# Optimization experiments

Hardware: AMD Instinct MI355X
Metric: run time of the kernel (lower is better)

## Reference

```python
import jax, jax.numpy as jnp
import numpy as np
import math

D_MODEL = 256
NUM_HEADS = 8
K_NEIGHBORS = 16


def sine_pos_embedding(pos_xy, d_model):
    # Faithful to PositionalEncoding: pos_xy [B, N, 2] -> [B, N, d_model]
    half = d_model // 2
    dim_t = jnp.arange(half, dtype=jnp.float32)
    dim_t = 10000.0 ** (2.0 * jnp.floor(dim_t / 2.0) / half)
    recip = (2.0 * math.pi) / dim_t  # [half]
    px = pos_xy[:, :, 0, None] * recip  # [B, N, half]
    py = pos_xy[:, :, 1, None] * recip
    def interleave(p):
        s = jnp.sin(p[:, :, 0::2])
        c = jnp.cos(p[:, :, 1::2])
        return jnp.stack((s, c), axis=3).reshape(p.shape[0], p.shape[1], -1)
    return jnp.concatenate((interleave(py), interleave(px)), axis=2)


def knn_indices(pos, K, valid_mask):
    # Faithful to find_k_nearest_neighbors: cdist, mask invalid ROWS with +inf, topk smallest.
    # pos: [B, N, 3], valid_mask: [B, N] -> indices [B, N, K]
    sq = jnp.sum(pos * pos, axis=-1)  # [B, N]
    d2 = sq[:, :, None] + sq[:, None, :] - 2.0 * jnp.einsum('bnd,bmd->bnm', pos, pos)
    dist = jnp.sqrt(jnp.maximum(d2, 0.0))  # [B, N, N]
    INF = jnp.float32(np.inf)
    dist = jnp.where(valid_mask[:, :, None], dist, INF)  # torch masks rows via (~mask).unsqueeze(-1)
    _, idx = jax.lax.top_k(-dist, K)  # smallest distances
    return idx  # [B, N, K] int32


def setup_inputs() -> dict:
    key = jax.random.key(0)
    ks = jax.random.split(key, 8)
    B, N, D = 16, 1024, D_MODEL
    x = jax.random.normal(ks[0], (B, N, D), dtype=jnp.float32)
    x_pos = jax.random.normal(ks[1], (B, N, 3), dtype=jnp.float32) * 50.0
    x_mask = jax.random.bernoulli(ks[2], 0.9, (B, N))
    # guarantee at least one valid token per batch row (module asserts sum > 0)
    x_mask = x_mask.at[:, 0].set(True)
    scale = 1.0 / math.sqrt(D)
    Wq = jax.random.normal(ks[3], (D, D), dtype=jnp.float32) * scale
    Wk = jax.random.normal(ks[4], (D, D), dtype=jnp.float32) * scale
    Wv = jax.random.normal(ks[5], (D, D), dtype=jnp.float32) * scale
    Wo = jax.random.normal(ks[6], (D, D), dtype=jnp.float32) * scale
    return {"x": x, "x_pos": x_pos, "x_mask": x_mask,
            "Wq": Wq, "Wk": Wk, "Wv": Wv, "Wo": Wo}


def local_attention(x, pe, valid, idx, Wq, Wk, Wv, Wo):
    B, N, D = x.shape
    H = NUM_HEADS
    dh = D // H
    q = (x + pe) @ Wq  # [B, N, D]
    k = (x + pe) @ Wk
    v = x @ Wv
    # gather K neighbors per query: [B, N, K, D]
    gather = jax.vmap(lambda arr, ii: arr[ii])
    k_n = gather(k, idx)
    v_n = gather(v, idx)
    nbr_valid = gather(valid, idx)  # [B, N, K]
    q = q.reshape(B, N, H, dh)
    k_n = k_n.reshape(B, N, K_NEIGHBORS, H, dh)
    v_n = v_n.reshape(B, N, K_NEIGHBORS, H, dh)
    scores = jnp.einsum('bnhd,bnkhd->bnhk', q, k_n) / math.sqrt(dh)
    scores = jnp.where(nbr_valid[:, :, None, :], scores, jnp.float32(-1e9))
    attn = jax.nn.softmax(scores, axis=-1)
    out = jnp.einsum('bnhk,bnkhd->bnhd', attn, v_n).reshape(B, N, D)
    out = out @ Wo
    out = x + out  # residual
    # zero out invalid tokens, as ret_full_feature is zeros for invalid rows
    return jnp.where(valid[:, :, None], out, 0.0)


def reference(x, x_pos, x_mask, Wq, Wk, Wv, Wo):
    idx = knn_indices(x_pos, K_NEIGHBORS, x_mask)
    pe = sine_pos_embedding(x_pos[:, :, 0:2], D_MODEL)
    pe = jnp.where(x_mask[:, :, None], pe, 0.0)
    return local_attention(x, pe, x_mask, idx, Wq, Wk, Wv, Wo)
```

## Files before the change

### kernel.cpp

```cpp
#include <hip/hip_runtime.h>
#include <math.h>

#define BB 16
#define NN 1024
#define DD 256
#define HH 8
#define DHH 32
#define KNBR 16
#define MM (BB*NN)

typedef __attribute__((ext_vector_type(8))) short  bf16x8;
typedef __attribute__((ext_vector_type(4))) float  f32x4;
typedef __attribute__((ext_vector_type(2))) unsigned short u16x2;
typedef __attribute__((ext_vector_type(4))) unsigned short u16x4;

#define OFF_FLAG 0
#define OFF_XPE  ((size_t)256)
#define OFF_XBF  (OFF_XPE + (size_t)MM*DD*2)
#define OFF_WT   (OFF_XBF + (size_t)MM*DD*2)
#define OFF_Q    (OFF_WT  + (size_t)4*DD*DD*2)
#define OFF_K    (OFF_Q   + (size_t)MM*DD*2)
#define OFF_V    (OFF_K   + (size_t)MM*DD*2)
#define OFF_AO   OFF_XPE
#define OFF_IDX  (OFF_V   + (size_t)MM*DD*2)
#define WS_NEED  (OFF_IDX + (size_t)MM*KNBR*4)

__device__ __forceinline__ float bf2f(unsigned short u) {
    unsigned x = ((unsigned)u) << 16;
    return __builtin_bit_cast(float, x);
}
__device__ __forceinline__ unsigned short f2bf(float f) {
    unsigned x = __builtin_bit_cast(unsigned, f);
    unsigned r = (x + 0x7fffu + ((x >> 16) & 1u)) >> 16;
    return (unsigned short)r;
}
__device__ __forceinline__ int mbcnt64(unsigned long long b) {
    return __builtin_amdgcn_mbcnt_hi((unsigned)(b >> 32),
           __builtin_amdgcn_mbcnt_lo((unsigned)b, 0));
}

__device__ __forceinline__ int get_valid(const void* m, int i, int u8) {
    if (u8) return ((const unsigned char*)m)[i] != 0;
    return ((const unsigned*)m)[i] != 0u;
}

__global__ __launch_bounds__(256, 8) void prep_fused(
    const float* __restrict__ xpos, int* __restrict__ idxout,
    const float* __restrict__ x, const void* __restrict__ mask,
    int* __restrict__ flag,
    const float* __restrict__ Wq, const float* __restrict__ Wk,
    const float* __restrict__ Wv, const float* __restrict__ Wo,
    unsigned short* __restrict__ WT,
    unsigned short* __restrict__ xpebf, unsigned short* __restrict__ xbf) {
    __shared__ float4   sp[NN];
    __shared__ unsigned scand[4][64];
    int bid = blockIdx.x;
    int tid = threadIdx.x;

    if (bid == 0) {
        __shared__ int s_u8, s_f32;
        if (tid == 0) { s_u8 = 0; s_f32 = 0; }
        __syncthreads();
        int u8 = 0, f32 = 0;
        const unsigned* mraw = (const unsigned*)mask;
        for (int i = tid; i < 4096; i += 256) {
            unsigned w = mraw[i];
            if (w == 0x3f800000u) f32 = 1;
            else if (w > 1u) u8 = 1;
        }
        if (u8)  atomicOr(&s_u8, 1);
        if (f32) atomicOr(&s_f32, 1);
        __syncthreads();
        if (tid == 0) *flag = (s_f32 ? 0 : (s_u8 ? 1 : 0));
        return;
    }
    if (bid >= 5121) {
        int pb = bid - 5121;
        int t = pb * 2 + (tid >> 7);
        int p = tid & 127;
        int half = p >> 6;
        int j = p & 63;
        float pos = xpos[(size_t)t*3 + (half ? 0 : 1)];
        float recip = 6.2831853071795864f * exp2f(-(float)j * 0.20762050593045952f);
        float th = pos * recip;
        float s, c;
        __sincosf(th, &s, &c);
        size_t o = (size_t)t*DD + half*128 + 2*j;
        float2 xv = *(const float2*)(x + o);
        u16x2 xb; xb[0] = f2bf(xv.x);     xb[1] = f2bf(xv.y);
        u16x2 xp; xp[0] = f2bf(xv.x + s); xp[1] = f2bf(xv.y + c);
        *(u16x2*)(xbf + o)   = xb;
        *(u16x2*)(xpebf + o) = xp;
        return;
    }
    if (bid >= 4097) {
        int g = bid - 4097;
        int wsel = g >> 8;
        int kk = g & 255;
        const float* W = (wsel == 0) ? Wq : (wsel == 1) ? Wk : (wsel == 2) ? Wv : Wo;
        WT[(size_t)wsel*65536 + (size_t)tid*256 + kk] = f2bf(W[(size_t)kk*256 + tid]);
        return;
    }

    int kb = bid - 1;
    int nblk = kb & 255;
    int b    = kb >> 8;
    for (int i = tid; i < NN; i += 256) {
        const float* p = xpos + ((size_t)b*NN + i)*3;
        float px = p[0], py = p[1], pz = p[2];
        sp[i] = make_float4(px, py, pz, px*px + py*py + pz*pz);
    }
    __syncthreads();
    int wave = tid >> 6, lane = tid & 63;
    int n = nblk * 4 + wave;
    float4 qp = sp[n];
    float d[16];
    #pragma unroll
    for (int t = 0; t < 16; ++t) {
        float4 pm = sp[lane + 64*t];
        float dot = qp.x*pm.x + qp.y*pm.y + qp.z*pm.z;
        float d2 = qp.w + pm.w - 2.f*dot;
        d[t] = fmaxf(d2, 0.f);
    }
    float lmin = d[0];
    #pragma unroll
    for (int t = 1; t < 16; ++t) lmin = fminf(lmin, d[t]);
    float xs = lmin;
    #pragma unroll
    for (int kk = 2; kk <= 64; kk <<= 1) {
        #pragma unroll
        for (int j = kk >> 1; j >= 1; j >>= 1) {
            float vv = __shfl_xor(xs, j);
            bool up = ((lane & kk) == 0);
            bool lower = ((lane & j) == 0);
            xs = (up == lower) ? fminf(xs, vv) : fmaxf(xs, vv);
        }
    }
    float tau = __shfl(xs, 15);
    int T = 0;
    #pragma unroll
    for (int t = 0; t < 16; ++t) T += (d[t] <= tau) ? 1 : 0;
    #pragma unroll
    for (int off = 1; off <= 32; off <<= 1) T += __shfl_xor(T, off);

    bool fast = (T <= 64);
    if (fast) {
        int base = 0;
        #pragma unroll
        for (int t = 0; t < 16; ++t) {
            bool c = (d[t] <= tau);
            unsigned long long bb = __ballot(c);
            if (c) scand[wave][base + mbcnt64(bb)] = __builtin_bit_cast(unsigned, d[t]);
            base += (int)__popcll(bb);
        }
    }
    __syncthreads();

    int out_base = (b*NN + n) * KNBR;
    if (fast) {
        unsigned key = (lane < T) ? scand[wave][lane] : 0xFFFFFFFFu;
        #pragma unroll
        for (int kk = 2; kk <= 64; kk <<= 1) {
            #pragma unroll
            for (int j = kk >> 1; j >= 1; j >>= 1) {
                unsigned vv = (unsigned)__shfl_xor((int)key, j);
                bool up = ((lane & kk) == 0);
                bool lower = ((lane & j) == 0);
                bool takemin = (up == lower);
                key = (takemin == (key < vv)) ? key : vv;
            }
        }
        unsigned tau2 = (unsigned)__shfl((int)key, 15);
        int c1 = (int)__popcll(__ballot(key < tau2));
        int lt_base = 0, eq_seen = 0;
        #pragma unroll
        for (int t = 0; t < 16; ++t) {
            unsigned du = __builtin_bit_cast(unsigned, d[t]);
            bool lt = du < tau2;
            bool eq = du == tau2;
            unsigned long long blt = __ballot(lt);
            unsigned long long beq = __ballot(beq ? eq : eq);
            (void)beq;
            beq = __ballot(eq);
            if (lt) idxout[out_base + lt_base + mbcnt64(blt)] = lane + 64*t;
            int er = eq_seen + mbcnt64(beq);
            if (eq && (c1 + er) < KNBR) idxout[out_base + c1 + er] = lane + 64*t;
            lt_base += (int)__popcll(blt);
            eq_seen += (int)__popcll(beq);
        }
    } else {
        #pragma unroll 1
        for (int it = 0; it < KNBR; ++it) {
            float bd = 3.4e38f; int bm = 1 << 30;
            #pragma unroll
            for (int t = 0; t < 16; ++t)
                if (d[t] < bd) { bd = d[t]; bm = lane + 64*t; }
            #pragma unroll
            for (int off = 32; off >= 1; off >>= 1) {
                float od = __shfl_xor(bd, off);
                int   om = __shfl_xor(bm, off);
                if (od < bd || (od == bd && om < bm)) { bd = od; bm = om; }
            }
            if (lane == 0) idxout[out_base + it] = bm;
            int sel = bm >> 6;
            int mine = ((bm & 63) == lane);
            #pragma unroll
            for (int t = 0; t < 16; ++t)
                if (mine && t == sel) d[t] = 3.4e38f;
        }
    }
}

template<int EPI>
__device__ __forceinline__ void gemm_mfma_core(
    const unsigned short* __restrict__ A, const unsigned short* __restrict__ BT,
    void* __restrict__ C, const float* __restrict__ resid,
    const void* __restrict__ mask, int u8, int bm, int bn, char* smem) {
    unsigned short (*As)[32] = (unsigned short (*)[32])smem;
    unsigned short (*Bs)[32] = (unsigned short (*)[32])(smem + 8192);
    int tid = threadIdx.x;
    int w = tid >> 6, l = tid & 63;
    int wr = w >> 1, wc = w & 1;

    f32x4 acc[4][4] = {};

    for (int kt = 0; kt < 8; ++kt) {
        #pragma unroll
        for (int j = 0; j < 2; ++j) {
            int c  = (w + j*4)*64 + l;
            int row = c >> 2;
            int cb  = (c & 3) * 16;
            const char* ga = (const char*)A + ((size_t)(bm + row)*256 + kt*32)*2 + cb;
            char* la = (char*)As + (size_t)(w + j*4)*1024;
            __builtin_amdgcn_global_load_lds(
                (const __attribute__((address_space(1))) unsigned*)ga,
                (__attribute__((address_space(3))) unsigned*)la, 16, 0, 0);
            const char* gb = (const char*)BT + ((size_t)(bn + row)*256 + kt*32)*2 + cb;
            char* lb = (char*)Bs + (size_t)(w + j*4)*1024;
            __builtin_amdgcn_global_load_lds(
                (const __attribute__((address_space(1))) unsigned*)gb,
                (__attribute__((address_space(3))) unsigned*)lb, 16, 0, 0);
        }
        __syncthreads();

        bf16x8 af[4], bfr[4];
        #pragma unroll
        for (int m = 0; m < 4; ++m)
            af[m] = *(const bf16x8*)&As[wr*64 + m*16 + (l & 15)][(l >> 4) * 8];
        #pragma unroll
        for (int n = 0; n < 4; ++n)
            bfr[n] = *(const bf16x8*)&Bs[wc*64 + n*16 + (l & 15)][(l >> 4) * 8];
        #pragma unroll
        for (int m = 0; m < 4; ++m)
            #pragma unroll
            for (int n = 0; n < 4; ++n)
                acc[m][n] = __builtin_amdgcn_mfma_f32_16x16x32_bf16(af[m], bfr[n], acc[m][n], 0, 0, 0);
        __syncthreads();
    }

    int colb = bn + wc*64 + (l & 15);
    #pragma unroll
    for (int m = 0; m < 4; ++m) {
        int row0 = bm + wr*64 + m*16 + (l >> 4)*4;
        #pragma unroll
        for (int r = 0; r < 4; ++r) {
            int row = row0 + r;
            int valid = 1;
            if (EPI) valid = get_valid(mask, row, u8);
            #pragma unroll
            for (int n = 0; n < 4; ++n) {
                int cc = colb + n*16;
                float val = acc[m][n][r];
                if (EPI) {
                    val = valid ? resid[(size_t)row*256 + cc] + val : 0.f;
                    ((float*)C)[(size_t)row*256 + cc] = val;
                } else {
                    ((unsigned short*)C)[(size_t)row*256 + cc] = f2bf(val);
                }
            }
        }
    }
}

__global__ __launch_bounds__(256) void gemm_qkv_mfma(
    const unsigned short* __restrict__ xpebf, const unsigned short* __restrict__ xbf,
    const unsigned short* __restrict__ WT,
    unsigned short* __restrict__ q, unsigned short* __restrict__ k,
    unsigned short* __restrict__ v) {
    __shared__ __align__(16) char smem[16384];
    int z = blockIdx.z;
    const unsigned short* A  = (z == 2) ? xbf : xpebf;
    const unsigned short* BT = WT + (size_t)z * 65536;
    unsigned short* C = (z == 0) ? q : (z == 1) ? k : v;
    gemm_mfma_core<0>(A, BT, C, nullptr, nullptr, 0, blockIdx.x*128, blockIdx.y*128, smem);
}

__global__ __launch_bounds__(256) void gemm_out_mfma(
    const unsigned short* __restrict__ aobf, const unsigned short* __restrict__ WT,
    const float* __restrict__ x, const void* __restrict__ mask,
    const int* __restrict__ flag, float* __restrict__ out) {
    __shared__ __align__(16) char smem[16384];
    int u8 = *flag;
    gemm_mfma_core<1>(aobf, WT + (size_t)3 * 65536, out, x, mask, u8,
                      blockIdx.x * 128, blockIdx.y * 128, smem);
}

__global__ __launch_bounds__(256) void attn_kernel(
    const unsigned short* __restrict__ q, const unsigned short* __restrict__ k,
    const unsigned short* __restrict__ v, const int* __restrict__ idx,
    const void* __restrict__ mask, const int* __restrict__ flag,
    unsigned short* __restrict__ aobf) {
    __shared__ int   s_j[4][16];
    __shared__ float s_w[4][16][8];
    int u8 = *flag;
    int wave = threadIdx.x >> 6, lane = threadIdx.x & 63;
    int cpx = gridDim.x >> 3;
    int sb = ((int)blockIdx.x & 7) * cpx + ((int)blockIdx.x >> 3);
    int t = sb * 4 + wave;
    int b = t >> 10;
    int sub = lane & 3, nbr = lane >> 2;
    int j = idx[(size_t)t*KNBR + nbr];
    if (lane < 16) s_j[wave][lane] = idx[(size_t)t*KNBR + lane];
    int nv = get_valid(mask, b*NN + j, u8);
    const unsigned short* qb = q + (size_t)t*DD;
    const unsigned short* kb = k + ((size_t)(b*NN + j))*DD;

    float w[8];
    #pragma unroll
    for (int h = 0; h < 8; ++h) {
        bf16x8 qv = *(const bf16x8*)(qb + h*32 + sub*8);
        bf16x8 kv = *(const bf16x8*)(kb + h*32 + sub*8);
        float acc = 0.f;
        #pragma unroll
        for (int e = 0; e < 8; ++e)
            acc += bf2f((unsigned short)qv[e]) * bf2f((unsigned short)kv[e]);
        acc += __shfl_xor(acc, 1);
        acc += __shfl_xor(acc, 2);
        float s = nv ? acc * 0.17677669529663688f : -1e9f;
        float m = s;
        #pragma unroll
        for (int off = 4; off <= 32; off <<= 1) m = fmaxf(m, __shfl_xor(m, off));
        float e = __expf(s - m);
        float sum = e;
        #pragma unroll
        for (int off = 4; off <= 32; off <<= 1) sum += __shfl_xor(sum, off);
        w[h] = e / sum;
    }
    if (sub == 0) {
        #pragma unroll
        for (int h = 0; h < 8; ++h) s_w[wave][nbr][h] = w[h];
    }
    __syncthreads();

    int c0 = lane * 4;
    int h = lane >> 3;
    float o0 = 0.f, o1 = 0.f, o2 = 0.f, o3 = 0.f;
    #pragma unroll
    for (int kk = 0; kk < 16; ++kk) {
        int jj = s_j[wave][kk];
        float wk = s_w[wave][kk][h];
        u16x4 vv = *(const u16x4*)(v + ((size_t)(b*NN + jj))*DD + c0);
        o0 += wk * bf2f(vv[0]);
        o1 += wk * bf2f(vv[1]);
        o2 += wk * bf2f(vv[2]);
        o3 += wk * bf2f(vv[3]);
    }
    u16x4 st;
    st[0] = f2bf(o0); st[1] = f2bf(o1); st[2] = f2bf(o2); st[3] = f2bf(o3);
    *(u16x4*)(aobf + (size_t)t*DD + c0) = st;
}

extern "C" void kernel_launch(void* const* d_in, const int* in_sizes, int n_in,
                              void* d_out, int out_size, void* d_ws, size_t ws_size,
                              hipStream_t stream) {
    const float* x    = (const float*)d_in[0];
    const float* xpos = (const float*)d_in[1];
    const void*  mask = d_in[2];
    const float* Wq   = (const float*)d_in[3];
    const float* Wk   = (const float*)d_in[4];
    const float* Wv   = (const float*)d_in[5];
    const float* Wo   = (const float*)d_in[6];
    float* out = (float*)d_out;
    char*  ws  = (char*)d_ws;
    if (ws_size < WS_NEED) return;

    int*            flag  = (int*)           (ws + OFF_FLAG);
    unsigned short* xpebf = (unsigned short*)(ws + OFF_XPE);
    unsigned short* xbf   = (unsigned short*)(ws + OFF_XBF);
    unsigned short* WT    = (unsigned short*)(ws + OFF_WT);
    unsigned short* q     = (unsigned short*)(ws + OFF_Q);
    unsigned short* k     = (unsigned short*)(ws + OFF_K);
    unsigned short* v     = (unsigned short*)(ws + OFF_V);
    unsigned short* aobf  = (unsigned short*)(ws + OFF_AO);
    int*            idx   = (int*)           (ws + OFF_IDX);

    prep_fused<<<13313, 256, 0, stream>>>(xpos, idx, x, mask, flag,
                                          Wq, Wk, Wv, Wo, WT, xpebf, xbf);
    gemm_qkv_mfma<<<dim3(128, 2, 3), 256, 0, stream>>>(xpebf, xbf, WT, q, k, v);
    attn_kernel<<<MM/4, 256, 0, stream>>>(q, k, v, idx, mask, flag, aobf);
    gemm_out_mfma<<<dim3(128, 2), 256, 0, stream>>>(aobf, WT, x, mask, flag, out);
}
```

Before: 80.91 us.

## Process two queries per wave in attention and remap GEMM block order

The attention kernel now has each wave handle two query tokens, interleaving their loads and shuffle reductions to raise memory-level parallelism. It also drops the __syncthreads, since each wave only reads its own shared slots. Both GEMM kernels switch to a 1D grid with a swizzled block-to-tile mapping intended to spread blocks across XCDs and improve L2 locality. A redundant ballot in the KNN selection is also removed. The extra per-wave work raises register pressure and halves the attention grid size.

```diff
diff --git a/kernel.cpp b/kernel.cpp
--- a/kernel.cpp
+++ b/kernel.cpp
@@ -179,9 +179,7 @@
             bool lt = du < tau2;
             bool eq = du == tau2;
             unsigned long long blt = __ballot(lt);
-            unsigned long long beq = __ballot(beq ? eq : eq);
-            (void)beq;
-            beq = __ballot(eq);
+            unsigned long long beq = __ballot(eq);
             if (lt) idxout[out_base + lt_base + mbcnt64(blt)] = lane + 64*t;
             int er = eq_seen + mbcnt64(beq);
             if (eq && (c1 + er) < KNBR) idxout[out_base + c1 + er] = lane + 64*t;
@@ -288,11 +286,16 @@
     unsigned short* __restrict__ q, unsigned short* __restrict__ k,
     unsigned short* __restrict__ v) {
     __shared__ __align__(16) char smem[16384];
-    int z = blockIdx.z;
-    const unsigned short* A  = (z == 2) ? xbf : xpebf;
-    const unsigned short* BT = WT + (size_t)z * 65536;
-    unsigned short* C = (z == 0) ? q : (z == 1) ? k : v;
-    gemm_mfma_core<0>(A, BT, C, nullptr, nullptr, 0, blockIdx.x*128, blockIdx.y*128, smem);
+    int bid = blockIdx.x;
+    int i   = bid >> 3;
+    int gx  = (bid & 7) * 16 + (i & 15);
+    int yz  = i >> 4;
+    int gy  = yz & 1;
+    int gz  = yz >> 1;
+    const unsigned short* A  = (gz == 2) ? xbf : xpebf;
+    const unsigned short* BT = WT + (size_t)gz * 65536;
+    unsigned short* C = (gz == 0) ? q : (gz == 1) ? k : v;
+    gemm_mfma_core<0>(A, BT, C, nullptr, nullptr, 0, gx*128, gy*128, smem);
 }
 
 __global__ __launch_bounds__(256) void gemm_out_mfma(
@@ -301,8 +304,12 @@
     const int* __restrict__ flag, float* __restrict__ out) {
     __shared__ __align__(16) char smem[16384];
     int u8 = *flag;
+    int bid = blockIdx.x;
+    int i   = bid >> 3;
+    int gx  = (bid & 7) * 16 + (i & 15);
+    int gy  = i >> 4;
     gemm_mfma_core<1>(aobf, WT + (size_t)3 * 65536, out, x, mask, u8,
-                      blockIdx.x * 128, blockIdx.y * 128, smem);
+                      gx * 128, gy * 128, smem);
 }
 
 __global__ __launch_bounds__(256) void attn_kernel(
@@ -310,64 +317,85 @@
     const unsigned short* __restrict__ v, const int* __restrict__ idx,
     const void* __restrict__ mask, const int* __restrict__ flag,
     unsigned short* __restrict__ aobf) {
-    __shared__ int   s_j[4][16];
-    __shared__ float s_w[4][16][8];
+    __shared__ int   s_j[4][2][16];
+    __shared__ float s_w[4][2][16][8];
     int u8 = *flag;
     int wave = threadIdx.x >> 6, lane = threadIdx.x & 63;
     int cpx = gridDim.x >> 3;
     int sb = ((int)blockIdx.x & 7) * cpx + ((int)blockIdx.x >> 3);
-    int t = sb * 4 + wave;
-    int b = t >> 10;
+    int t0 = sb * 8 + wave * 2;
+    int b = t0 >> 10;
     int sub = lane & 3, nbr = lane >> 2;
-    int j = idx[(size_t)t*KNBR + nbr];
-    if (lane < 16) s_j[wave][lane] = idx[(size_t)t*KNBR + lane];
-    int nv = get_valid(mask, b*NN + j, u8);
-    const unsigned short* qb = q + (size_t)t*DD;
-    const unsigned short* kb = k + ((size_t)(b*NN + j))*DD;
-
-    float w[8];
+    int j0 = idx[(size_t)t0*KNBR + nbr];
+    int j1 = idx[(size_t)(t0+1)*KNBR + nbr];
+    if (lane < 16) {
+        s_j[wave][0][lane] = idx[(size_t)t0*KNBR + lane];
+        s_j[wave][1][lane] = idx[(size_t)(t0+1)*KNBR + lane];
+    }
+    int nv0 = get_valid(mask, b*NN + j0, u8);
+    int nv1 = get_valid(mask, b*NN + j1, u8);
+    const unsigned short* qb0 = q + (size_t)t0*DD;
+    const unsigned short* qb1 = qb0 + DD;
+    const unsigned short* kb0 = k + ((size_t)(b*NN + j0))*DD;
+    const unsigned short* kb1 = k + ((size_t)(b*NN + j1))*DD;
+
     #pragma unroll
     for (int h = 0; h < 8; ++h) {
-        bf16x8 qv = *(const bf16x8*)(qb + h*32 + sub*8);
-        bf16x8 kv = *(const bf16x8*)(kb + h*32 + sub*8);
-        float acc = 0.f;
-        #pragma unroll
-        for (int e = 0; e < 8; ++e)
-            acc += bf2f((unsigned short)qv[e]) * bf2f((unsigned short)kv[e]);
-        acc += __shfl_xor(acc, 1);
-        acc += __shfl_xor(acc, 2);
-        float s = nv ? acc * 0.17677669529663688f : -1e9f;
-        float m = s;
-        #pragma unroll
-        for (int off = 4; off <= 32; off <<= 1) m = fmaxf(m, __shfl_xor(m, off));
-        float e = __expf(s - m);
-        float sum = e;
-        #pragma unroll
-        for (int off = 4; off <= 32; off <<= 1) sum += __shfl_xor(sum, off);
-        w[h] = e / sum;
-    }
-    if (sub == 0) {
-        #pragma unroll
-        for (int h = 0; h < 8; ++h) s_w[wave][nbr][h] = w[h];
-    }
-    __syncthreads();
+        bf16x8 qv0 = *(const bf16x8*)(qb0 + h*32 + sub*8);
+        bf16x8 kv0 = *(const bf16x8*)(kb0 + h*32 + sub*8);
+        bf16x8 qv1 = *(const bf16x8*)(qb1 + h*32 + sub*8);
+        bf16x8 kv1 = *(const bf16x8*)(kb1 + h*32 + sub*8);
+        float a0 = 0.f, a1 = 0.f;
+        #pragma unroll
+        for (int e = 0; e < 8; ++e) {
+            a0 += bf2f((unsigned short)qv0[e]) * bf2f((unsigned short)kv0[e]);
+            a1 += bf2f((unsigned short)qv1[e]) * bf2f((unsigned short)kv1[e]);
+        }
+        a0 += __shfl_xor(a0, 1);  a1 += __shfl_xor(a1, 1);
+        a0 += __shfl_xor(a0, 2);  a1 += __shfl_xor(a1, 2);
+        float s0 = nv0 ? a0 * 0.17677669529663688f : -1e9f;
+        float s1 = nv1 ? a1 * 0.17677669529663688f : -1e9f;
+        float m0 = s0, m1 = s1;
+        #pragma unroll
+        for (int off = 4; off <= 32; off <<= 1) {
+            m0 = fmaxf(m0, __shfl_xor(m0, off));
+            m1 = fmaxf(m1, __shfl_xor(m1, off));
+        }
+        float e0 = __expf(s0 - m0), e1 = __expf(s1 - m1);
+        float u0 = e0, u1 = e1;
+        #pragma unroll
+        for (int off = 4; off <= 32; off <<= 1) {
+            u0 += __shfl_xor(u0, off);
+            u1 += __shfl_xor(u1, off);
+        }
+        if (sub == 0) {
+            s_w[wave][0][nbr][h] = e0 / u0;
+            s_w[wave][1][nbr][h] = e1 / u1;
+        }
+    }
 
     int c0 = lane * 4;
     int h = lane >> 3;
-    float o0 = 0.f, o1 = 0.f, o2 = 0.f, o3 = 0.f;
+    float o0a = 0.f, o0b = 0.f, o0c = 0.f, o0d = 0.f;
+    float o1a = 0.f, o1b = 0.f, o1c = 0.f, o1d = 0.f;
     #pragma unroll
     for (int kk = 0; kk < 16; ++kk) {
-        int jj = s_j[wave][kk];
-        float wk = s_w[wave][kk][h];
-        u16x4 vv = *(const u16x4*)(v + ((size_t)(b*NN + jj))*DD + c0);
-        o0 += wk * bf2f(vv[0]);
-        o1 += wk * bf2f(vv[1]);
-        o2 += wk * bf2f(vv[2]);
-        o3 += wk * bf2f(vv[3]);
-    }
-    u16x4 st;
-    st[0] = f2bf(o0); st[1] = f2bf(o1); st[2] = f2bf(o2); st[3] = f2bf(o3);
-    *(u16x4*)(aobf + (size_t)t*DD + c0) = st;
+        int ja = s_j[wave][0][kk];
+        int jb = s_j[wave][1][kk];
+        float wa = s_w[wave][0][kk][h];
+        float wb = s_w[wave][1][kk][h];
+        u16x4 va = *(const u16x4*)(v + ((size_t)(b*NN + ja))*DD + c0);
+        u16x4 vb = *(const u16x4*)(v + ((size_t)(b*NN + jb))*DD + c0);
+        o0a += wa * bf2f(va[0]); o0b += wa * bf2f(va[1]);
+        o0c += wa * bf2f(va[2]); o0d += wa * bf2f(va[3]);
+        o1a += wb * bf2f(vb[0]); o1b += wb * bf2f(vb[1]);
+        o1c += wb * bf2f(vb[2]); o1d += wb * bf2f(vb[3]);
+    }
+    u16x4 st0, st1;
+    st0[0] = f2bf(o0a); st0[1] = f2bf(o0b); st0[2] = f2bf(o0c); st0[3] = f2bf(o0d);
+    st1[0] = f2bf(o1a); st1[1] = f2bf(o1b); st1[2] = f2bf(o1c); st1[3] = f2bf(o1d);
+    *(u16x4*)(aobf + (size_t)t0*DD + c0)       = st0;
+    *(u16x4*)(aobf + (size_t)(t0+1)*DD + c0)   = st1;
 }
 
 extern "C" void kernel_launch(void* const* d_in, const int* in_sizes, int n_in,
@@ -396,7 +424,7 @@
 
     prep_fused<<<13313, 256, 0, stream>>>(xpos, idx, x, mask, flag,
                                           Wq, Wk, Wv, Wo, WT, xpebf, xbf);
-    gemm_qkv_mfma<<<dim3(128, 2, 3), 256, 0, stream>>>(xpebf, xbf, WT, q, k, v);
-    attn_kernel<<<MM/4, 256, 0, stream>>>(q, k, v, idx, mask, flag, aobf);
-    gemm_out_mfma<<<dim3(128, 2), 256, 0, stream>>>(aobf, WT, x, mask, flag, out);
-}
+    gemm_qkv_mfma<<<768, 256, 0, stream>>>(xpebf, xbf, WT, q, k, v);
+    attn_kernel<<<MM/8, 256, 0, stream>>>(q, k, v, idx, mask, flag, aobf);
+    gemm_out_mfma<<<256, 256, 0, stream>>>(aobf, WT, x, mask, flag, out);
+}
```

Result: no change. 82.36 us (+1.8%).
